# Kernel tuning notes

Measured on AMD Instinct MI355X. Metric: run time of the kernel, lower is better.

Reference implementation:

```python
import jax, jax.numpy as jnp
import numpy as np
from jax import lax

H_IMG, W_IMG = 1280, 1280
STRIDES = (8, 16, 32, 64, 128)
FEAT_SHAPES = tuple((H_IMG // s) * (W_IMG // s) for s in STRIDES)  # (25600,6400,1600,400,100)
N_POINTS = sum(FEAT_SHAPES)  # 34100
NUM_CLASSES = 1
TOPK = 1000
SCORE_THRESH = 0.05
NMS_THRESH = 0.5
MAX_DET = 300
BATCH = 8
N_GT = 200


def make_points():
    # matches AnchorFreePS.reference_points: cell centers at stride*i + stride//2, (cx, cy) order
    pts = []
    for s in STRIDES:
        h, w = H_IMG // s, W_IMG // s
        cx = np.arange(w, dtype=np.float32) * s + s // 2
        cy = np.arange(h, dtype=np.float32) * s + s // 2
        gy, gx = np.meshgrid(cy, cx, indexing='ij')
        pts.append(np.stack([gx, gy], axis=-1).reshape(-1, 2))
    return jnp.asarray(np.concatenate(pts, axis=0))


def setup_inputs() -> dict:
    key = jax.random.key(0)
    k1, k2, k3, k4 = jax.random.split(key, 4)
    points = make_points()  # [N,2]
    xy = jax.random.uniform(k1, (BATCH, N_GT, 2), minval=0.0, maxval=1000.0)
    wh = jax.random.uniform(k2, (BATCH, N_GT, 2), minval=20.0, maxval=260.0)
    gt_boxes = jnp.concatenate([xy, xy + wh], axis=-1)  # [B,M,4] x1y1x2y2
    cls_logits = jax.random.normal(k3, (BATCH, N_POINTS, NUM_CLASSES)) * 1.5 - 3.0
    regression = jax.random.uniform(k4, (BATCH, N_POINTS, 4)) * 0.1  # normalized ltrb codes
    return {"points": points, "gt_boxes": gt_boxes, "cls_logits": cls_logits, "regression": regression}


def match_points_to_boxes(points, gt_boxes):
    # point-in-box test + area-cost argmin (compute_loss matched_idxs)
    px = points[None, :, None, 0]  # [1,N,1]
    py = points[None, :, None, 1]
    b = gt_boxes[:, None, :, :]    # [B,1,M,4]
    inside = (px >= b[..., 0]) & (px <= b[..., 2]) & (py >= b[..., 1]) & (py <= b[..., 3])  # [B,N,M]
    matched = jnp.any(inside, axis=-1)  # [B,N]
    areas = (gt_boxes[..., 2] - gt_boxes[..., 0]) * (gt_boxes[..., 3] - gt_boxes[..., 1])  # [B,M]
    BIG = jnp.float32(2 ** 31 - 1)  # torch.iinfo(torch.int).max
    cost = jnp.where(inside, areas[:, None, :], BIG)
    idx = jnp.argmin(cost, axis=-1)
    return jnp.where(matched, idx, -1)


def decode_boxes(rel, pts):
    # FCOSBoxCoder.decode_single with weights (1,1,1,1)
    l = rel[:, 0] * W_IMG
    t = rel[:, 1] * H_IMG
    r = rel[:, 2] * W_IMG
    b = rel[:, 3] * H_IMG
    x, y = pts[:, 0], pts[:, 1]
    return jnp.stack([x - l, y - t, x + r, y + b], axis=-1)


def clip_boxes(boxes):
    return jnp.stack([
        jnp.clip(boxes[:, 0], 0.0, W_IMG),
        jnp.clip(boxes[:, 1], 0.0, H_IMG),
        jnp.clip(boxes[:, 2], 0.0, W_IMG),
        jnp.clip(boxes[:, 3], 0.0, H_IMG)], axis=-1)


def nms(boxes, scores, labels, valid_init):
    # fixed-size sequential NMS equivalent to batched_nms (same-label suppression)
    work = lax.stop_gradient(jnp.where(valid_init, scores, -jnp.inf))

    def body(w, _):
        i = jnp.argmax(w)
        s = w[i]
        box = boxes[i]
        x1 = jnp.maximum(box[0], boxes[:, 0])
        y1 = jnp.maximum(box[1], boxes[:, 1])
        x2 = jnp.minimum(box[2], boxes[:, 2])
        y2 = jnp.minimum(box[3], boxes[:, 3])
        inter = jnp.clip(x2 - x1, 0.0) * jnp.clip(y2 - y1, 0.0)
        a1 = (box[2] - box[0]) * (box[3] - box[1])
        a2 = (boxes[:, 2] - boxes[:, 0]) * (boxes[:, 3] - boxes[:, 1])
        iou = inter / (a1 + a2 - inter + 1e-9)
        supp = (iou > NMS_THRESH) & (labels == labels[i])
        w = jnp.where(supp, -jnp.inf, w).at[i].set(-jnp.inf)
        return w, (i, s)

    _, (idxs, picked) = lax.scan(body, work, None, length=MAX_DET)
    valid = picked > -jnp.inf
    return idxs, valid


def postprocess_image(points, cls_i, reg_i):
    bx_list, sc_list, lb_list = [], [], []
    off = 0
    for size in FEAT_SHAPES:  # fixed small level loop
        sl = slice(off, off + size)
        off += size
        scores = jax.nn.sigmoid(cls_i[sl]).reshape(-1)  # [size*C]
        k = min(TOPK, size * NUM_CLASSES)
        sc, idx = lax.top_k(scores, k)
        a = idx // NUM_CLASSES
        lb = idx % NUM_CLASSES
        bx = clip_boxes(decode_boxes(reg_i[sl][a], points[sl][a]))
        bx_list.append(bx)
        sc_list.append(sc)
        lb_list.append(lb)
    boxes = jnp.concatenate(bx_list, axis=0)
    scores = jnp.concatenate(sc_list, axis=0)
    labels = jnp.concatenate(lb_list, axis=0)
    idxs, valid = nms(boxes, scores, labels, scores > SCORE_THRESH)
    out_boxes = jnp.where(valid[:, None], boxes[idxs], 0.0)
    out_scores = jnp.where(valid, scores[idxs], 0.0)
    out_labels = jnp.where(valid, labels[idxs], -1)
    return out_boxes, out_scores, out_labels, valid


def reference(points, gt_boxes, cls_logits, regression):
    matched_idxs = match_points_to_boxes(points, gt_boxes)  # [B,N]
    boxes, scores, labels, valid = jax.vmap(
        lambda c, r: postprocess_image(points, c, r))(cls_logits, regression)
    return matched_idxs, boxes, scores, labels, valid
```

## Files before the change

### kernel.cpp

```cpp
#include <hip/hip_runtime.h>
#include <stdint.h>

#define N_POINTS   34100
#define BATCH      8
#define N_GT       200
#define NLEV       5
#define NCAND      3500
#define MAX_DET    300
#define SCORE_TH   0.05f
#define NMS_TH     0.5f
#define IMG        1280.0f
#define NBIN       4096
#define TIE_CAP    4096
#define MTH 0.50000002980232238769531250

#define OUT_MATCH  0
#define OUT_BOXES  272800
#define OUT_SCORES 282400
#define OUT_LABELS 284800
#define OUT_VALID  287200

#define WS_KEYS    0
#define WS_PARAMS  1746560
#define WS_SBOX    2632192
#define WS_SSC     3080192
#define WS_MASK    3192192
#define WS_DIAG    9500032
#define MASK_STRIDE 98560
#define DIAG_STRIDE 3520

typedef unsigned long long u64;
typedef uint32_t u32;

__device__ __forceinline__ int mask_off(int c) {
    int g = c >> 6;
    return 64 * (55 * g - (g * (g - 1)) / 2) + (c - (g << 6)) * (55 - g);
}
__device__ __forceinline__ int level_of(int p) {
    return (p < 25600) ? 0 : (p < 32000) ? 1 : (p < 33600) ? 2 : (p < 34000) ? 3 : 4;
}
__device__ __forceinline__ int loff_of(int l) {
    return (l == 0) ? 0 : (l == 1) ? 25600 : (l == 2) ? 32000 : (l == 3) ? 33600 : 34000;
}
__device__ __forceinline__ int lsize_of(int l) {
    return (l == 0) ? 25600 : (l == 1) ? 6400 : (l == 2) ? 1600 : (l == 3) ? 400 : 100;
}
__device__ __forceinline__ int k_of(int l) {
    return (l == 0) ? 1000 : (l == 1) ? 1000 : (l == 2) ? 1000 : (l == 3) ? 400 : 100;
}
__device__ __forceinline__ u64 readlane64(u64 v, int t) {
    u32 lo = (u32)__builtin_amdgcn_readlane((int)(u32)v, t);
    u32 hi = (u32)__builtin_amdgcn_readlane((int)(u32)(v >> 32), t);
    return ((u64)hi << 32) | lo;
}

#define MPT 2
#define MATCH_BLKS 536
#define FRONT_BLKS (MATCH_BLKS + BATCH * NLEV)

__global__ __launch_bounds__(256)
void front_kernel(const float* __restrict__ points,
                  const float* __restrict__ gt,
                  const float* __restrict__ logits,
                  float* __restrict__ out_match,
                  u32* __restrict__ keys,
                  u32* __restrict__ params) {
#pragma clang fp contract(off)
    __shared__ __align__(16) u32 shm[NBIN];
    const int tid = threadIdx.x;

    if (blockIdx.x < MATCH_BLKS) {
        float* bx1 = (float*)shm;
        float* by1 = bx1 + 256;
        float* bx2 = bx1 + 512;
        float* by2 = bx1 + 768;
        float* ar  = bx1 + 1024;
        const int b = blockIdx.x / 67;
        const int chunk = blockIdx.x - b * 67;
        const int base = chunk * (256 * MPT) + tid;

        for (int j = tid; j < N_GT; j += 256) {
            float x1 = gt[(b * N_GT + j) * 4 + 0];
            float y1 = gt[(b * N_GT + j) * 4 + 1];
            float x2 = gt[(b * N_GT + j) * 4 + 2];
            float y2 = gt[(b * N_GT + j) * 4 + 3];
            bx1[j] = x1; by1[j] = y1; bx2[j] = x2; by2[j] = y2;
            ar[j] = (x2 - x1) * (y2 - y1);
        }
        __syncthreads();

        const float BIGF = 2147483648.0f;
        float px[MPT], py[MPT], best[MPT];
        int bi[MPT];
#pragma unroll
        for (int k = 0; k < MPT; ++k) {
            int p = base + k * 256;
            int pc = (p < N_POINTS) ? p : 0;
            px[k] = points[pc * 2 + 0];
            py[k] = points[pc * 2 + 1];
            best[k] = BIGF; bi[k] = -1;
        }
        for (int j = 0; j < N_GT; ++j) {
            float x1 = bx1[j], y1 = by1[j], x2 = bx2[j], y2 = by2[j], a = ar[j];
#pragma unroll
            for (int k = 0; k < MPT; ++k) {
                bool inside = (px[k] >= x1) && (px[k] <= x2) &&
                              (py[k] >= y1) && (py[k] <= y2);
                float cost = inside ? a : BIGF;
                if (cost < best[k]) { best[k] = cost; bi[k] = j; }
            }
        }
#pragma unroll
        for (int k = 0; k < MPT; ++k) {
            int p = base + k * 256;
            if (p < N_POINTS) out_match[b * N_POINTS + p] = (float)bi[k];
        }
    } else {
        const int seg = blockIdx.x - MATCH_BLKS;
        const int b = seg / NLEV;
        const int l = seg - b * NLEV;
        const int lane = tid & 63;

        for (int i = tid; i < NBIN; i += 256) shm[i] = 0u;
        __syncthreads();

        const float* lg = logits + b * N_POINTS + loff_of(l);
        u32* kout = keys + b * N_POINTS + loff_of(l);
        const int n = lsize_of(l);
        for (int i = tid; i < n; i += 256) {
            float s = 1.0f / (1.0f + expf(-lg[i]));
            u32 u = __float_as_uint(s);
            u32 key = (u & 0x80000000u) ? ~u : (u | 0x80000000u);
            kout[i] = key;
            atomicAdd(&shm[(key >> 19) & 4095u], 1u);
        }
        __syncthreads();

        if (tid < 64) {
            const u32 K = (u32)k_of(l);
            u32 S = 0;
#pragma unroll 8
            for (int i = 0; i < 64; ++i) S += shm[lane * 64 + i];
            u32 acc = S;
#pragma unroll
            for (int off = 1; off < 64; off <<= 1) {
                u32 v = (u32)__shfl_down((int)acc, off);
                if (lane + off < 64) acc += v;
            }
            u32 sfxAfter = acc - S;
            bool hit = (sfxAfter < K) && (sfxAfter + S >= K);
            u64 bal = __ballot(hit);
            int Lg = (int)__builtin_ctzll(bal);
            u32 sfxG = (u32)__shfl((int)sfxAfter, Lg);

            u32 v = shm[Lg * 64 + lane];
            u32 acc2 = v;
#pragma unroll
            for (int off = 1; off < 64; off <<= 1) {
                u32 t = (u32)__shfl_down((int)acc2, off);
                if (lane + off < 64) acc2 += t;
            }
            u32 sfx2 = sfxG + acc2 - v;
            bool hit2 = (sfx2 < K) && (sfx2 + v >= K);
            if (hit2) {
                params[seg * 2 + 0] = (u32)(Lg * 64 + lane);
                params[seg * 2 + 1] = K - sfx2;
            }
        }
    }
}

#define SORT_T 1024
__global__ __launch_bounds__(SORT_T)
void pipeline_kernel(const u32* __restrict__ keys,
                     const u32* __restrict__ params,
                     const float* __restrict__ reg,
                     const float* __restrict__ points,
                     float* __restrict__ sboxes,
                     float* __restrict__ sscores) {
#pragma clang fp contract(off)
    __shared__ u64 sk[4096];
    __shared__ u64 tb[TIE_CAP];
    __shared__ u64 aux[4096];
    __shared__ u32 h[NBIN];
    __shared__ u32 bs[NBIN];
    __shared__ u32 sTl[NLEV], skkl[NLEV], wt[16];
    __shared__ u32 scnt, stcnt;

    const int b = blockIdx.x;
    const int tid = threadIdx.x;
    const int lane = tid & 63;
    const int wid = tid >> 6;
    const u32* kk_ = keys + b * N_POINTS;

    if (tid < NLEV) {
        sTl[tid]  = params[(b * NLEV + tid) * 2 + 0];
        skkl[tid] = params[(b * NLEV + tid) * 2 + 1];
    }
    if (tid == 0) { scnt = 0u; stcnt = 0u; }
    __syncthreads();

    const int NPAIR = N_POINTS / 2;
    for (int i0 = tid; i0 - tid < NPAIR; i0 += SORT_T) {
        bool act = i0 < NPAIR;
        int p0 = act ? (2 * i0) : 0;
        int p1 = p0 + 1;
        u32 key0 = kk_[p0], key1 = kk_[p1];
        int l0 = level_of(p0), l1 = level_of(p1);
        u32 d0 = (key0 >> 19) & 4095u, d1 = (key1 >> 19) & 4095u;
        u32 T0 = sTl[l0], T1 = sTl[l1];
        bool def0 = act && (d0 > T0), def1 = act && (d1 > T1);
        bool tie0 = act && (d0 == T0), tie1 = act && (d1 == T1);
        u64 k0 = ((u64)key0 << 18) | ((u64)(7 - l0) << 15)
               | (u64)(32767 - (p0 - loff_of(l0)));
        u64 k1 = ((u64)key1 << 18) | ((u64)(7 - l1) << 15)
               | (u64)(32767 - (p1 - loff_of(l1)));

        u32 nd = (u32)def0 + (u32)def1;
        u32 pre = nd;
#pragma unroll
        for (int off = 1; off < 64; off <<= 1) {
            u32 v = (u32)__shfl_up((int)pre, off);
            if (lane >= off) pre += v;
        }
        u32 base_ = 0;
        if (lane == 63 && pre) base_ = atomicAdd(&scnt, pre);
        base_ = (u32)__shfl((int)base_, 63);
        u32 ex = pre - nd;
        if (def0) sk[base_ + ex] = k0;
        if (def1) sk[base_ + ex + (u32)def0] = k1;

        u32 nt = (u32)tie0 + (u32)tie1;
        u32 pret = nt;
#pragma unroll
        for (int off = 1; off < 64; off <<= 1) {
            u32 v = (u32)__shfl_up((int)pret, off);
            if (lane >= off) pret += v;
        }
        u32 baset = 0;
        if (lane == 63 && pret) baset = atomicAdd(&stcnt, pret);
        baset = (u32)__shfl((int)baset, 63);
        u32 ext = pret - nt;
        if (tie0 && baset + ext < TIE_CAP) tb[baset + ext] = k0;
        if (tie1 && baset + ext + (u32)tie0 < TIE_CAP)
            tb[baset + ext + (u32)tie0] = k1;
    }
    __syncthreads();

    const u64 below = (lane == 0) ? 0ull : (~0ull >> (64 - lane));
    int t = (int)stcnt; if (t > TIE_CAP) t = TIE_CAP;
    for (int j0 = tid; j0 - tid < t; j0 += SORT_T) {
        bool active = j0 < t;
        u64 kj = active ? tb[j0] : 0ull;
        u32 lvtag = (u32)(kj >> 15) & 7u;
        int r = 0;
        for (int i = 0; i < t; ++i) {
            u64 ki = tb[i];
            r += (ki > kj && (((u32)(ki >> 15) & 7u) == lvtag)) ? 1 : 0;
        }
        bool inc = active && (r < (int)skkl[7 - lvtag]);
        u64 grp = __ballot(inc);
        if (grp) {
            int leader = (int)__builtin_ctzll(grp);
            u32 base_ = 0;
            if (lane == leader)
                base_ = atomicAdd(&scnt, (u32)__builtin_popcountll(grp));
            base_ = (u32)__shfl((int)base_, leader);
            if (inc) sk[base_ + (u32)__builtin_popcountll(grp & below)] = kj;
        }
    }
    __syncthreads();
    const int total = (int)scnt;

    for (int i = tid; i < NBIN; i += SORT_T) h[i] = 0u;
    __syncthreads();
    for (int i = tid; i < total; i += SORT_T)
        atomicAdd(&h[(u32)(sk[i] >> 37) & 4095u], 1u);
    __syncthreads();

    u32 t0 = h[4095 - 4 * tid];
    u32 t1 = h[4095 - (4 * tid + 1)];
    u32 t2 = h[4095 - (4 * tid + 2)];
    u32 t3 = h[4095 - (4 * tid + 3)];
    u32 tsum = t0 + t1 + t2 + t3;
    u32 sc_ = tsum;
#pragma unroll
    for (int off = 1; off < 64; off <<= 1) {
        u32 v = (u32)__shfl_up((int)sc_, off);
        if (lane >= off) sc_ += v;
    }
    if (lane == 63) wt[wid] = sc_;
    __syncthreads();
    if (tid < 64) {
        u32 v = (tid < 16) ? wt[tid] : 0u;
        u32 s2 = v;
#pragma unroll
        for (int off = 1; off < 16; off <<= 1) {
            u32 x = (u32)__shfl_up((int)s2, off);
            if (tid >= off) s2 += x;
        }
        if (tid < 16) wt[tid] = s2 - v;
    }
    __syncthreads();
    u32 run = (sc_ - tsum) + wt[wid];
    bs[4095 - 4 * tid] = run;       run += t0;
    bs[4095 - (4 * tid + 1)] = run; run += t1;
    bs[4095 - (4 * tid + 2)] = run; run += t2;
    bs[4095 - (4 * tid + 3)] = run;
    __syncthreads();
    for (int i = tid; i < NBIN; i += SORT_T) h[i] = 0u;
    __syncthreads();
    for (int i = tid; i < total; i += SORT_T) {
        u64 k = sk[i];
        u32 d = (u32)(k >> 37) & 4095u;
        u32 pos = bs[d] + atomicAdd(&h[d], 1u);
        aux[pos] = k;
    }
    __syncthreads();
    for (int p = tid; p < total; p += SORT_T) {
        u64 kp = aux[p];
        u32 d = (u32)(kp >> 37) & 4095u;
        u32 gbase = bs[d];
        u32 gend = (d == 0) ? (u32)total : bs[d - 1];
        u32 r = 0;
        for (u32 q = gbase; q < gend; ++q) r += (aux[q] > kp) ? 1u : 0u;
        sk[gbase + r] = kp;
    }
    __syncthreads();

    for (int r = tid; r < NCAND; r += SORT_T) {
        float x1 = 0.f, y1 = 0.f, x2 = 0.f, y2 = 0.f, sc = 0.f;
        if (r < total) {
            u64 k50 = sk[r];
            int lowb = (int)(k50 & 0x3FFFFull);
            int l = 7 - (lowb >> 15);
            int idxl = 32767 - (lowb & 32767);
            int p = loff_of(l) + idxl;
            u32 key32 = (u32)(k50 >> 18);
            sc = __uint_as_float(key32 ^ 0x80000000u);
            int gp = b * N_POINTS + p;
            float l_ = reg[gp * 4 + 0] * IMG;
            float t_ = reg[gp * 4 + 1] * IMG;
            float r_ = reg[gp * 4 + 2] * IMG;
            float bb = reg[gp * 4 + 3] * IMG;
            float px = points[p * 2 + 0];
            float py = points[p * 2 + 1];
            x1 = fminf(fmaxf(px - l_, 0.0f), IMG);
            y1 = fminf(fmaxf(py - t_, 0.0f), IMG);
            x2 = fminf(fmaxf(px + r_, 0.0f), IMG);
            y2 = fminf(fmaxf(py + bb, 0.0f), IMG);
        }
        int slot = b * NCAND + r;
        sboxes[slot * 4 + 0] = x1;
        sboxes[slot * 4 + 1] = y1;
        sboxes[slot * 4 + 2] = x2;
        sboxes[slot * 4 + 3] = y2;
        sscores[slot] = sc;
    }
}

__global__ __launch_bounds__(256)
void mask_kernel(const float* __restrict__ sboxes,
                 const float* __restrict__ sscores,
                 u64* __restrict__ mask,
                 u64* __restrict__ diag) {
#pragma clang fp contract(off)
    const int b = blockIdx.y;
    const int wv = threadIdx.x >> 6;
    const int lane = threadIdx.x & 63;
    const int NG = (NCAND + 3) >> 2;
    const int NH = (NG + 1) >> 1;
    const int gidx = blockIdx.x * 4 + wv;
    if (gidx >= NH) return;

    const float4* gb = (const float4*)sboxes + b * NCAND;
    const float* gs = sscores + b * NCAND;
    u64* mout = mask + (size_t)b * MASK_STRIDE;
    u64* dout = diag + (size_t)b * DIAG_STRIDE;

    for (int s = 0; s < 2; ++s) {
        const int g0 = (s == 0) ? gidx : (NG - 1 - gidx);
        if (s == 1 && g0 == gidx) break;
        const int c0 = g0 << 2;

        float4 bc[4]; float a1[4]; bool ok[4]; int g[4]; u64* rp[4];
        bool any = false;
#pragma unroll
        for (int i = 0; i < 4; ++i) {
            int c = c0 + i;
            int cc = (c < NCAND) ? c : (NCAND - 1);
            bc[i] = gb[cc];
            a1[i] = (bc[i].z - bc[i].x) * (bc[i].w - bc[i].y);
            ok[i] = (c < NCAND) && (gs[cc] > SCORE_TH);
            g[i] = cc >> 6;
            rp[i] = mout + mask_off(cc) - g[i];
            any |= ok[i];
        }
        if (!any) continue;

        for (int w = (c0 >> 6); w < 55; ++w) {
            int cj = (w << 6) + lane;
            float4 bj = (cj < NCAND) ? gb[cj] : make_float4(0.f, 0.f, 0.f, 0.f);
            float a2 = (bj.z - bj.x) * (bj.w - bj.y);
#pragma unroll
            for (int i = 0; i < 4; ++i) {
                float x1 = fmaxf(bc[i].x, bj.x);
                float y1 = fmaxf(bc[i].y, bj.y);
                float x2 = fminf(bc[i].z, bj.z);
                float y2 = fminf(bc[i].w, bj.w);
                float inter = fmaxf(x2 - x1, 0.f) * fmaxf(y2 - y1, 0.f);
                float denom = a1[i] + a2 - inter + 1e-9f;
                float hf = 0.5f * denom;
                float rr = fmaf(0x1p-25f, denom, hf);
                u64 bits = __ballot(inter > rr);
                u64 eq = __ballot(inter == rr);
                if (eq) {
                    u64 fb = __ballot((double)inter > MTH * (double)denom);
                    bits |= (eq & fb);
                }
                if (lane == 0 && ok[i] && w >= g[i]) {
                    rp[i][w] = bits;
                    if (w == g[i]) dout[c0 + i] = bits;
                }
            }
        }
    }
}

__global__ __launch_bounds__(64)
void scan_kernel(const float* __restrict__ sboxes,
                 const float* __restrict__ sscores,
                 const u64* __restrict__ mask,
                 const u64* __restrict__ diag,
                 float* __restrict__ out) {
    const int b = blockIdx.x;
    const int lane = threadIdx.x;
    const float4* gb = (const float4*)sboxes + b * NCAND;
    const float* gs = sscores + b * NCAND;
    const u64* mrow = mask + (size_t)b * MASK_STRIDE;
    const u64* drow = diag + (size_t)b * DIAG_STRIDE;

    float* ob = out + OUT_BOXES  + b * MAX_DET * 4;
    float* os = out + OUT_SCORES + b * MAX_DET;
    float* ol = out + OUT_LABELS + b * MAX_DET;
    float* ov = out + OUT_VALID  + b * MAX_DET;

    u64 m = 0ull;
    u64 rowN = drow[lane];
    float4 bjN = gb[lane];
    float sjN = gs[lane];

    int kept = 0;
    for (int w = 0; w < 55; ++w) {
        const int wbase = w << 6;
        const u64 row = rowN;
        const float4 bj = bjN;
        const float sj = sjN;
        if (w < 54) {
            int cn = wbase + 64 + lane;
            int cc = (cn < NCAND) ? cn : (NCAND - 1);
            rowN = drow[cc];
            bjN = gb[cc];
            float s = gs[cc];
            sjN = (cn < NCAND) ? s : 0.f;
        }
        int c = wbase + lane;
        u64 bad = __ballot(!((c < NCAND) && (sj > SCORE_TH)));
        u64 cur = readlane64(m, w) | bad;
        u64 km = 0ull;
        while (kept < MAX_DET) {
            u64 avail = ~cur;
            if (avail == 0ull) break;
            int t = (int)__builtin_ctzll(avail);
            u64 r = readlane64(row, t);
            cur |= r | (1ull << t);
            km |= 1ull << t;
            if (lane == t) {
                ob[kept * 4 + 0] = bj.x;
                ob[kept * 4 + 1] = bj.y;
                ob[kept * 4 + 2] = bj.z;
                ob[kept * 4 + 3] = bj.w;
                os[kept] = sj;
                ol[kept] = 0.0f;
                ov[kept] = 1.0f;
            }
            kept++;
        }
        if (km) {
            const bool lr = (lane >= w && lane < 55);
            const int lo = lane - w;
            u64 acc = 0ull;
            while (km) {
#define POPBIT(tn) int tn = -1; if (km) { tn = (int)__builtin_ctzll(km); km &= km - 1ull; }
                POPBIT(t0) POPBIT(t1) POPBIT(t2) POPBIT(t3)
                POPBIT(t4) POPBIT(t5) POPBIT(t6) POPBIT(t7)
#undef POPBIT
                u64 v0 = 0, v1 = 0, v2 = 0, v3 = 0, v4 = 0, v5 = 0, v6 = 0, v7 = 0;
                if (lr) {
                    v0 = mrow[mask_off(wbase + t0) + lo];
                    if (t1 >= 0) v1 = mrow[mask_off(wbase + t1) + lo];
                    if (t2 >= 0) v2 = mrow[mask_off(wbase + t2) + lo];
                    if (t3 >= 0) v3 = mrow[mask_off(wbase + t3) + lo];
                    if (t4 >= 0) v4 = mrow[mask_off(wbase + t4) + lo];
                    if (t5 >= 0) v5 = mrow[mask_off(wbase + t5) + lo];
                    if (t6 >= 0) v6 = mrow[mask_off(wbase + t6) + lo];
                    if (t7 >= 0) v7 = mrow[mask_off(wbase + t7) + lo];
                }
                acc |= ((v0 | v1) | (v2 | v3)) | ((v4 | v5) | (v6 | v7));
            }
            m |= acc;
        }
        if (kept >= MAX_DET) break;
    }
    for (int k = kept + lane; k < MAX_DET; k += 64) {
        ob[k * 4 + 0] = 0.f; ob[k * 4 + 1] = 0.f;
        ob[k * 4 + 2] = 0.f; ob[k * 4 + 3] = 0.f;
        os[k] = 0.f; ol[k] = -1.f; ov[k] = 0.f;
    }
}

extern "C" void kernel_launch(void* const* d_in, const int* in_sizes, int n_in,
                              void* d_out, int out_size, void* d_ws, size_t ws_size,
                              hipStream_t stream) {
    const float* points = (const float*)d_in[0];
    const float* gt     = (const float*)d_in[1];
    const float* logits = (const float*)d_in[2];
    const float* reg    = (const float*)d_in[3];
    float* out = (float*)d_out;

    u32* keys      = (u32*)((char*)d_ws + WS_KEYS);
    u32* params    = (u32*)((char*)d_ws + WS_PARAMS);
    float* sboxes  = (float*)((char*)d_ws + WS_SBOX);
    float* sscores = (float*)((char*)d_ws + WS_SSC);
    u64* mask   = (u64*)((char*)d_ws + WS_MASK);
    u64* diag   = (u64*)((char*)d_ws + WS_DIAG);

    front_kernel<<<FRONT_BLKS, 256, 0, stream>>>(points, gt, logits,
                                                 out + OUT_MATCH, keys, params);

    pipeline_kernel<<<BATCH, SORT_T, 0, stream>>>(keys, params, reg, points,
                                                  sboxes, sscores);

    dim3 g5((((NCAND + 3) / 4 + 1) / 2 + 3) / 4, BATCH);
    mask_kernel<<<g5, 256, 0, stream>>>(sboxes, sscores, mask, diag);

    scan_kernel<<<BATCH, 64, 0, stream>>>(sboxes, sscores, mask, diag, out);
}
```

Before: 270.7 us.

## Fuse NMS mask and scan kernels with per-image atomic counter handoff

Merges the IoU mask kernel and the greedy scan kernel into one launch. Extra blocks, one per image, spin on a per-image counter that mask blocks increment when they finish, then run the scan. The counter is reset in the front kernel. This removes one kernel launch and the global barrier between them, so an image's scan can start as soon as its own mask rows are done. The cost is spin-waiting blocks and reliance on all mask blocks being co-resident or scheduled ahead of the waiters, which could deadlock or stall.

```diff
diff --git a/kernel.cpp b/kernel.cpp
--- a/kernel.cpp
+++ b/kernel.cpp
@@ -22,6 +22,7 @@
 
 #define WS_KEYS    0
 #define WS_PARAMS  1746560
+#define WS_SYNC    1747200
 #define WS_SBOX    2632192
 #define WS_SSC     3080192
 #define WS_MASK    3192192
@@ -29,6 +30,9 @@
 #define MASK_STRIDE 98560
 #define DIAG_STRIDE 3520
 
+#define MASK_BLKS_PER_IMG 110
+#define MASK_BLKS_TOT     (MASK_BLKS_PER_IMG * BATCH)
+
 typedef unsigned long long u64;
 typedef uint32_t u32;
 
@@ -64,7 +68,8 @@
                   const float* __restrict__ logits,
                   float* __restrict__ out_match,
                   u32* __restrict__ keys,
-                  u32* __restrict__ params) {
+                  u32* __restrict__ params,
+                  u32* __restrict__ sync_) {
 #pragma clang fp contract(off)
     __shared__ __align__(16) u32 shm[NBIN];
     const int tid = threadIdx.x;
@@ -120,6 +125,8 @@
         const int b = seg / NLEV;
         const int l = seg - b * NLEV;
         const int lane = tid & 63;
+
+        if (seg == 0 && tid < 16) sync_[tid] = 0u;
 
         for (int i = tid; i < NBIN; i += 256) shm[i] = 0u;
         __syncthreads();
@@ -360,163 +367,181 @@
 }
 
 __global__ __launch_bounds__(256)
-void mask_kernel(const float* __restrict__ sboxes,
-                 const float* __restrict__ sscores,
-                 u64* __restrict__ mask,
-                 u64* __restrict__ diag) {
+void masknms_kernel(const float* __restrict__ sboxes,
+                    const float* __restrict__ sscores,
+                    u64* __restrict__ mask,
+                    u64* __restrict__ diag,
+                    u32* __restrict__ sync_,
+                    float* __restrict__ out) {
 #pragma clang fp contract(off)
-    const int b = blockIdx.y;
-    const int wv = threadIdx.x >> 6;
-    const int lane = threadIdx.x & 63;
+    const int tid = threadIdx.x;
+    const int lane = tid & 63;
+
+    if (blockIdx.x >= MASK_BLKS_TOT) {
+        if (tid >= 64) return;
+        const int b = blockIdx.x - MASK_BLKS_TOT;
+        u32 it = 0;
+        while (__hip_atomic_load(&sync_[8 + b], __ATOMIC_RELAXED,
+                                 __HIP_MEMORY_SCOPE_AGENT)
+                   < (u32)MASK_BLKS_PER_IMG && it < (1u << 26)) {
+            __builtin_amdgcn_s_sleep(32);
+            ++it;
+        }
+        __threadfence();
+
+        const float4* gb = (const float4*)sboxes + b * NCAND;
+        const float* gs = sscores + b * NCAND;
+        const u64* mrow = mask + (size_t)b * MASK_STRIDE;
+        const u64* drow = diag + (size_t)b * DIAG_STRIDE;
+
+        float* ob = out + OUT_BOXES  + b * MAX_DET * 4;
+        float* os = out + OUT_SCORES + b * MAX_DET;
+        float* ol = out + OUT_LABELS + b * MAX_DET;
+        float* ov = out + OUT_VALID  + b * MAX_DET;
+
+        u64 m = 0ull;
+        u64 rowN = drow[lane];
+        float4 bjN = gb[lane];
+        float sjN = gs[lane];
+
+        int kept = 0;
+        for (int w = 0; w < 55; ++w) {
+            const int wbase = w << 6;
+            const u64 row = rowN;
+            const float4 bj = bjN;
+            const float sj = sjN;
+            if (w < 54) {
+                int cn = wbase + 64 + lane;
+                int cc = (cn < NCAND) ? cn : (NCAND - 1);
+                rowN = drow[cc];
+                bjN = gb[cc];
+                float s = gs[cc];
+                sjN = (cn < NCAND) ? s : 0.f;
+            }
+            int c = wbase + lane;
+            u64 bad = __ballot(!((c < NCAND) && (sj > SCORE_TH)));
+            u64 cur = readlane64(m, w) | bad;
+            u64 km = 0ull;
+            while (kept < MAX_DET) {
+                u64 avail = ~cur;
+                if (avail == 0ull) break;
+                int t = (int)__builtin_ctzll(avail);
+                u64 r = readlane64(row, t);
+                cur |= r | (1ull << t);
+                km |= 1ull << t;
+                if (lane == t) {
+                    ob[kept * 4 + 0] = bj.x;
+                    ob[kept * 4 + 1] = bj.y;
+                    ob[kept * 4 + 2] = bj.z;
+                    ob[kept * 4 + 3] = bj.w;
+                    os[kept] = sj;
+                    ol[kept] = 0.0f;
+                    ov[kept] = 1.0f;
+                }
+                kept++;
+            }
+            if (km) {
+                const bool lr = (lane >= w && lane < 55);
+                const int lo = lane - w;
+                u64 acc = 0ull;
+                while (km) {
+#define POPBIT(tn) int tn = -1; if (km) { tn = (int)__builtin_ctzll(km); km &= km - 1ull; }
+                    POPBIT(t0) POPBIT(t1) POPBIT(t2) POPBIT(t3)
+                    POPBIT(t4) POPBIT(t5) POPBIT(t6) POPBIT(t7)
+#undef POPBIT
+                    u64 v0 = 0, v1 = 0, v2 = 0, v3 = 0, v4 = 0, v5 = 0, v6 = 0, v7 = 0;
+                    if (lr) {
+                        v0 = mrow[mask_off(wbase + t0) + lo];
+                        if (t1 >= 0) v1 = mrow[mask_off(wbase + t1) + lo];
+                        if (t2 >= 0) v2 = mrow[mask_off(wbase + t2) + lo];
+                        if (t3 >= 0) v3 = mrow[mask_off(wbase + t3) + lo];
+                        if (t4 >= 0) v4 = mrow[mask_off(wbase + t4) + lo];
+                        if (t5 >= 0) v5 = mrow[mask_off(wbase + t5) + lo];
+                        if (t6 >= 0) v6 = mrow[mask_off(wbase + t6) + lo];
+                        if (t7 >= 0) v7 = mrow[mask_off(wbase + t7) + lo];
+                    }
+                    acc |= ((v0 | v1) | (v2 | v3)) | ((v4 | v5) | (v6 | v7));
+                }
+                m |= acc;
+            }
+            if (kept >= MAX_DET) break;
+        }
+        for (int k = kept + lane; k < MAX_DET; k += 64) {
+            ob[k * 4 + 0] = 0.f; ob[k * 4 + 1] = 0.f;
+            ob[k * 4 + 2] = 0.f; ob[k * 4 + 3] = 0.f;
+            os[k] = 0.f; ol[k] = -1.f; ov[k] = 0.f;
+        }
+        return;
+    }
+
+    const int b = blockIdx.x / MASK_BLKS_PER_IMG;
+    const int gx = blockIdx.x - b * MASK_BLKS_PER_IMG;
+    const int wv = tid >> 6;
     const int NG = (NCAND + 3) >> 2;
     const int NH = (NG + 1) >> 1;
-    const int gidx = blockIdx.x * 4 + wv;
-    if (gidx >= NH) return;
+    const int gidx = gx * 4 + wv;
 
     const float4* gb = (const float4*)sboxes + b * NCAND;
     const float* gs = sscores + b * NCAND;
     u64* mout = mask + (size_t)b * MASK_STRIDE;
     u64* dout = diag + (size_t)b * DIAG_STRIDE;
 
-    for (int s = 0; s < 2; ++s) {
-        const int g0 = (s == 0) ? gidx : (NG - 1 - gidx);
-        if (s == 1 && g0 == gidx) break;
-        const int c0 = g0 << 2;
-
-        float4 bc[4]; float a1[4]; bool ok[4]; int g[4]; u64* rp[4];
-        bool any = false;
-#pragma unroll
-        for (int i = 0; i < 4; ++i) {
-            int c = c0 + i;
-            int cc = (c < NCAND) ? c : (NCAND - 1);
-            bc[i] = gb[cc];
-            a1[i] = (bc[i].z - bc[i].x) * (bc[i].w - bc[i].y);
-            ok[i] = (c < NCAND) && (gs[cc] > SCORE_TH);
-            g[i] = cc >> 6;
-            rp[i] = mout + mask_off(cc) - g[i];
-            any |= ok[i];
-        }
-        if (!any) continue;
-
-        for (int w = (c0 >> 6); w < 55; ++w) {
-            int cj = (w << 6) + lane;
-            float4 bj = (cj < NCAND) ? gb[cj] : make_float4(0.f, 0.f, 0.f, 0.f);
-            float a2 = (bj.z - bj.x) * (bj.w - bj.y);
+    if (gidx < NH) {
+        for (int s = 0; s < 2; ++s) {
+            const int g0 = (s == 0) ? gidx : (NG - 1 - gidx);
+            if (s == 1 && g0 == gidx) break;
+            const int c0 = g0 << 2;
+
+            float4 bc[4]; float a1[4]; bool ok[4]; int g[4]; u64* rp[4];
+            bool any = false;
 #pragma unroll
             for (int i = 0; i < 4; ++i) {
-                float x1 = fmaxf(bc[i].x, bj.x);
-                float y1 = fmaxf(bc[i].y, bj.y);
-                float x2 = fminf(bc[i].z, bj.z);
-                float y2 = fminf(bc[i].w, bj.w);
-                float inter = fmaxf(x2 - x1, 0.f) * fmaxf(y2 - y1, 0.f);
-                float denom = a1[i] + a2 - inter + 1e-9f;
-                float hf = 0.5f * denom;
-                float rr = fmaf(0x1p-25f, denom, hf);
-                u64 bits = __ballot(inter > rr);
-                u64 eq = __ballot(inter == rr);
-                if (eq) {
-                    u64 fb = __ballot((double)inter > MTH * (double)denom);
-                    bits |= (eq & fb);
+                int c = c0 + i;
+                int cc = (c < NCAND) ? c : (NCAND - 1);
+                bc[i] = gb[cc];
+                a1[i] = (bc[i].z - bc[i].x) * (bc[i].w - bc[i].y);
+                ok[i] = (c < NCAND) && (gs[cc] > SCORE_TH);
+                g[i] = cc >> 6;
+                rp[i] = mout + mask_off(cc) - g[i];
+                any |= ok[i];
+            }
+            if (!any) continue;
+
+            for (int w = (c0 >> 6); w < 55; ++w) {
+                int cj = (w << 6) + lane;
+                float4 bj = (cj < NCAND) ? gb[cj]
+                                         : make_float4(0.f, 0.f, 0.f, 0.f);
+                float a2 = (bj.z - bj.x) * (bj.w - bj.y);
+#pragma unroll
+                for (int i = 0; i < 4; ++i) {
+                    float x1 = fmaxf(bc[i].x, bj.x);
+                    float y1 = fmaxf(bc[i].y, bj.y);
+                    float x2 = fminf(bc[i].z, bj.z);
+                    float y2 = fminf(bc[i].w, bj.w);
+                    float inter = fmaxf(x2 - x1, 0.f) * fmaxf(y2 - y1, 0.f);
+                    float denom = a1[i] + a2 - inter + 1e-9f;
+                    float hf = 0.5f * denom;
+                    float rr = fmaf(0x1p-25f, denom, hf);
+                    u64 bits = __ballot(inter > rr);
+                    u64 eq = __ballot(inter == rr);
+                    if (eq) {
+                        u64 fb = __ballot((double)inter > MTH * (double)denom);
+                        bits |= (eq & fb);
+                    }
+                    if (lane == 0 && ok[i] && w >= g[i]) {
+                        __hip_atomic_store(&rp[i][w], bits, __ATOMIC_RELAXED,
+                                           __HIP_MEMORY_SCOPE_AGENT);
+                        if (w == g[i])
+                            __hip_atomic_store(&dout[c0 + i], bits,
+                                               __ATOMIC_RELAXED,
+                                               __HIP_MEMORY_SCOPE_AGENT);
+                    }
                 }
-                if (lane == 0 && ok[i] && w >= g[i]) {
-                    rp[i][w] = bits;
-                    if (w == g[i]) dout[c0 + i] = bits;
-                }
-            }
-        }
-    }
-}
-
-__global__ __launch_bounds__(64)
-void scan_kernel(const float* __restrict__ sboxes,
-                 const float* __restrict__ sscores,
-                 const u64* __restrict__ mask,
-                 const u64* __restrict__ diag,
-                 float* __restrict__ out) {
-    const int b = blockIdx.x;
-    const int lane = threadIdx.x;
-    const float4* gb = (const float4*)sboxes + b * NCAND;
-    const float* gs = sscores + b * NCAND;
-    const u64* mrow = mask + (size_t)b * MASK_STRIDE;
-    const u64* drow = diag + (size_t)b * DIAG_STRIDE;
-
-    float* ob = out + OUT_BOXES  + b * MAX_DET * 4;
-    float* os = out + OUT_SCORES + b * MAX_DET;
-    float* ol = out + OUT_LABELS + b * MAX_DET;
-    float* ov = out + OUT_VALID  + b * MAX_DET;
-
-    u64 m = 0ull;
-    u64 rowN = drow[lane];
-    float4 bjN = gb[lane];
-    float sjN = gs[lane];
-
-    int kept = 0;
-    for (int w = 0; w < 55; ++w) {
-        const int wbase = w << 6;
-        const u64 row = rowN;
-        const float4 bj = bjN;
-        const float sj = sjN;
-        if (w < 54) {
-            int cn = wbase + 64 + lane;
-            int cc = (cn < NCAND) ? cn : (NCAND - 1);
-            rowN = drow[cc];
-            bjN = gb[cc];
-            float s = gs[cc];
-            sjN = (cn < NCAND) ? s : 0.f;
-        }
-        int c = wbase + lane;
-        u64 bad = __ballot(!((c < NCAND) && (sj > SCORE_TH)));
-        u64 cur = readlane64(m, w) | bad;
-        u64 km = 0ull;
-        while (kept < MAX_DET) {
-            u64 avail = ~cur;
-            if (avail == 0ull) break;
-            int t = (int)__builtin_ctzll(avail);
-            u64 r = readlane64(row, t);
-            cur |= r | (1ull << t);
-            km |= 1ull << t;
-            if (lane == t) {
-                ob[kept * 4 + 0] = bj.x;
-                ob[kept * 4 + 1] = bj.y;
-                ob[kept * 4 + 2] = bj.z;
-                ob[kept * 4 + 3] = bj.w;
-                os[kept] = sj;
-                ol[kept] = 0.0f;
-                ov[kept] = 1.0f;
-            }
-            kept++;
-        }
-        if (km) {
-            const bool lr = (lane >= w && lane < 55);
-            const int lo = lane - w;
-            u64 acc = 0ull;
-            while (km) {
-#define POPBIT(tn) int tn = -1; if (km) { tn = (int)__builtin_ctzll(km); km &= km - 1ull; }
-                POPBIT(t0) POPBIT(t1) POPBIT(t2) POPBIT(t3)
-                POPBIT(t4) POPBIT(t5) POPBIT(t6) POPBIT(t7)
-#undef POPBIT
-                u64 v0 = 0, v1 = 0, v2 = 0, v3 = 0, v4 = 0, v5 = 0, v6 = 0, v7 = 0;
-                if (lr) {
-                    v0 = mrow[mask_off(wbase + t0) + lo];
-                    if (t1 >= 0) v1 = mrow[mask_off(wbase + t1) + lo];
-                    if (t2 >= 0) v2 = mrow[mask_off(wbase + t2) + lo];
-                    if (t3 >= 0) v3 = mrow[mask_off(wbase + t3) + lo];
-                    if (t4 >= 0) v4 = mrow[mask_off(wbase + t4) + lo];
-                    if (t5 >= 0) v5 = mrow[mask_off(wbase + t5) + lo];
-                    if (t6 >= 0) v6 = mrow[mask_off(wbase + t6) + lo];
-                    if (t7 >= 0) v7 = mrow[mask_off(wbase + t7) + lo];
-                }
-                acc |= ((v0 | v1) | (v2 | v3)) | ((v4 | v5) | (v6 | v7));
-            }
-            m |= acc;
-        }
-        if (kept >= MAX_DET) break;
-    }
-    for (int k = kept + lane; k < MAX_DET; k += 64) {
-        ob[k * 4 + 0] = 0.f; ob[k * 4 + 1] = 0.f;
-        ob[k * 4 + 2] = 0.f; ob[k * 4 + 3] = 0.f;
-        os[k] = 0.f; ol[k] = -1.f; ov[k] = 0.f;
-    }
+            }
+        }
+    }
+    __syncthreads();
+    if (tid == 0) atomicAdd(&sync_[8 + b], 1u);
 }
 
 extern "C" void kernel_launch(void* const* d_in, const int* in_sizes, int n_in,
@@ -530,19 +555,19 @@
 
     u32* keys      = (u32*)((char*)d_ws + WS_KEYS);
     u32* params    = (u32*)((char*)d_ws + WS_PARAMS);
+    u32* sync_     = (u32*)((char*)d_ws + WS_SYNC);
     float* sboxes  = (float*)((char*)d_ws + WS_SBOX);
     float* sscores = (float*)((char*)d_ws + WS_SSC);
     u64* mask   = (u64*)((char*)d_ws + WS_MASK);
     u64* diag   = (u64*)((char*)d_ws + WS_DIAG);
 
     front_kernel<<<FRONT_BLKS, 256, 0, stream>>>(points, gt, logits,
-                                                 out + OUT_MATCH, keys, params);
+                                                 out + OUT_MATCH, keys, params,
+                                                 sync_);
 
     pipeline_kernel<<<BATCH, SORT_T, 0, stream>>>(keys, params, reg, points,
                                                   sboxes, sscores);
 
-    dim3 g5((((NCAND + 3) / 4 + 1) / 2 + 3) / 4, BATCH);
-    mask_kernel<<<g5, 256, 0, stream>>>(sboxes, sscores, mask, diag);
-
-    scan_kernel<<<BATCH, 64, 0, stream>>>(sboxes, sscores, mask, diag, out);
-}
+    masknms_kernel<<<MASK_BLKS_TOT + BATCH, 256, 0, stream>>>(
+        sboxes, sscores, mask, diag, sync_, out);
+}
```

After: 275.5 us. No clear change (+1.8%).
